# Performance work log

Measured on AMD Instinct MI355X. Metric: run time of the kernel, lower is better.

Reference implementation:

```python
import jax, jax.numpy as jnp
import numpy as np
import math

BS, LQ, LKV = 4, 2048, 2048
D_LATENT, D_MODEL, HEADS = 512, 512, 8
D_K = D_MODEL // HEADS


def setup_inputs() -> dict:
    key = jax.random.key(0)
    ks = jax.random.split(key, 12)
    s = 0.02
    return {
        "q": jax.random.normal(ks[0], (BS, LQ, D_LATENT), jnp.float32),
        "k": jax.random.normal(ks[1], (BS, LKV, D_MODEL), jnp.float32),
        "v": jax.random.normal(ks[2], (BS, LKV, D_MODEL), jnp.float32),
        "weights": jax.random.uniform(ks[3], (BS, LKV), jnp.float32) + 1e-3,
        "Wq": jax.random.normal(ks[4], (D_LATENT, D_MODEL), jnp.float32) * s,
        "bq": jnp.zeros((D_MODEL,), jnp.float32),
        "Wk": jax.random.normal(ks[5], (D_MODEL, D_MODEL), jnp.float32) * s,
        "bk": jnp.zeros((D_MODEL,), jnp.float32),
        "Wv": jax.random.normal(ks[6], (D_MODEL, D_MODEL), jnp.float32) * s,
        "bv": jnp.zeros((D_MODEL,), jnp.float32),
        "Wo": jax.random.normal(ks[7], (D_MODEL, D_MODEL), jnp.float32) * s,
        "bo": jnp.zeros((D_MODEL,), jnp.float32),
    }


def reference(q, k, v, weights, Wq, bq, Wk, bk, Wv, bv, Wo, bo):
    bs = q.shape[0]
    # QKV projections, split into heads: [bs, h, L, d_k]
    qh = (q @ Wq + bq).reshape(bs, -1, HEADS, D_K).transpose(0, 2, 1, 3)
    kh = (k @ Wk + bk).reshape(bs, -1, HEADS, D_K).transpose(0, 2, 1, 3)
    vh = (v @ Wv + bv).reshape(bs, -1, HEADS, D_K).transpose(0, 2, 1, 3)
    # scaled dot-product scores [bs, h, Lq, Lkv]
    scores = jnp.einsum("bhqd,bhkd->bhqk", qh, kh) / math.sqrt(D_K)
    p = jax.nn.softmax(scores, axis=-1)
    # post-softmax external weight renormalization
    wp = p * weights[:, None, None, :]
    wp = wp / wp.sum(-1, keepdims=True)
    out = jnp.einsum("bhqk,bhkd->bhqd", wp, vh)
    concat = out.transpose(0, 2, 1, 3).reshape(bs, -1, D_MODEL)
    return concat @ Wo + bo
```

## Files before the change

### kernel.cpp

```cpp
#include <hip/hip_runtime.h>
#include <hip/hip_bf16.h>

#define LQ 2048
#define LKV 2048
#define DM 512
#define NH 8
#define DK 64

typedef __attribute__((ext_vector_type(8))) __bf16 bf16x8;
typedef __attribute__((ext_vector_type(4))) float f32x4;
typedef __attribute__((ext_vector_type(16))) float f32x16;

#define AS1 __attribute__((address_space(1)))
#define AS3 __attribute__((address_space(3)))

static __device__ __forceinline__ unsigned short f2bf(float x) {
  unsigned u = __float_as_uint(x);
  return (unsigned short)((u + 0x7fffu + ((u >> 16) & 1u)) >> 16);
}
static __device__ __forceinline__ float bf2f(unsigned short u) {
  return __uint_as_float(((unsigned)u) << 16);
}
static __device__ __forceinline__ bf16x8 cvt8(f32x4 a, f32x4 b) {
  bf16x8 r;
  r[0] = (__bf16)a[0]; r[1] = (__bf16)a[1]; r[2] = (__bf16)a[2]; r[3] = (__bf16)a[3];
  r[4] = (__bf16)b[0]; r[5] = (__bf16)b[1]; r[6] = (__bf16)b[2]; r[7] = (__bf16)b[3];
  return r;
}

__global__ __launch_bounds__(256) void transpose_w(
    const float* __restrict__ Wq, const float* __restrict__ Wk,
    const float* __restrict__ Wv, const float* __restrict__ Wo,
    unsigned short* __restrict__ WtAll)
{
  const float* W = blockIdx.z == 0 ? Wq : blockIdx.z == 1 ? Wk : blockIdx.z == 2 ? Wv : Wo;
  unsigned short* Wt = WtAll + (size_t)blockIdx.z * DM * DM;
  __shared__ float tile[32][33];
  const int t = threadIdx.x;
  const int tr = t >> 3;
  const int tc4 = (t & 7) * 4;
  const int k0 = blockIdx.x * 32, n0 = blockIdx.y * 32;
  float4 v = *(const float4*)(W + (size_t)(k0 + tr) * DM + n0 + tc4);
  tile[tr][tc4 + 0] = v.x; tile[tr][tc4 + 1] = v.y;
  tile[tr][tc4 + 2] = v.z; tile[tr][tc4 + 3] = v.w;
  __syncthreads();
  ushort4 o;
  o.x = f2bf(tile[tc4 + 0][tr]);
  o.y = f2bf(tile[tc4 + 1][tr]);
  o.z = f2bf(tile[tc4 + 2][tr]);
  o.w = f2bf(tile[tc4 + 3][tr]);
  *(ushort4*)(Wt + (size_t)(n0 + tr) * DM + k0 + tc4) = o;
}

__global__ __launch_bounds__(256) void gemm_qkv(
    const float* __restrict__ qin, const float* __restrict__ kin, const float* __restrict__ vin,
    const unsigned short* __restrict__ WtAll,
    const float* __restrict__ bq, const float* __restrict__ bk, const float* __restrict__ bv,
    unsigned short* __restrict__ qh, unsigned short* __restrict__ kh, unsigned short* __restrict__ vh)
{
  const int bid = blockIdx.x;
  const int x = bid & 7, j = bid >> 3;
  const int p = x + 8 * (j >> 2);
  const int nt = j & 3;
  const int mode = p >> 6, mtile = p & 63;

  const float* A = mode == 0 ? qin : (mode == 1 ? kin : vin);
  const unsigned short* Bt = WtAll + (size_t)mode * DM * DM;
  const float* bias = mode == 0 ? bq : (mode == 1 ? bk : bv);
  unsigned short* out = mode == 0 ? qh : (mode == 1 ? kh : vh);
  const float scale = (mode == 0) ? 0.18033688011112042f : 1.0f;

  __shared__ __align__(16) float As[128 * 32];
  __shared__ __align__(16) unsigned short Bs[128 * 32];

  const int tid = threadIdx.x;
  const int lane = tid & 63;
  const int w = tid >> 6;
  const int wr = w >> 1, wc = w & 1;
  const int l15 = lane & 15, g = lane >> 4;
  const int m0 = mtile * 128, n0 = nt * 128;

  f32x4 acc[4][4] = {};

  for (int k0 = 0; k0 < DM; k0 += 32) {
#pragma unroll
    for (int i = 0; i < 4; ++i) {
      int c = tid + i * 256;
      int row = c >> 3, slot = c & 7;
      const float* src = A + (size_t)(m0 + row) * DM + k0 + ((slot ^ (row & 7)) << 2);
      __builtin_amdgcn_global_load_lds((const AS1 unsigned*)src,
                                       (AS3 unsigned*)((char*)As + c * 16), 16, 0, 0);
    }
#pragma unroll
    for (int i = 0; i < 2; ++i) {
      int c = tid + i * 256;
      int row = c >> 2, slot = c & 3;
      const unsigned short* src = Bt + (size_t)(n0 + row) * DM + k0 + ((slot ^ ((row >> 1) & 3)) * 8);
      __builtin_amdgcn_global_load_lds((const AS1 unsigned*)src,
                                       (AS3 unsigned*)((char*)Bs + c * 16), 16, 0, 0);
    }
    __syncthreads();

    bf16x8 af[4], bfr[4];
#pragma unroll
    for (int mi = 0; mi < 4; ++mi) {
      int row = wr * 64 + mi * 16 + l15;
      f32x4 a0 = *(const f32x4*)((const char*)As + row * 128 + (((2 * g) ^ (row & 7)) << 4));
      f32x4 a1 = *(const f32x4*)((const char*)As + row * 128 + (((2 * g + 1) ^ (row & 7)) << 4));
      af[mi] = cvt8(a0, a1);
    }
#pragma unroll
    for (int ni = 0; ni < 4; ++ni) {
      int row = wc * 64 + ni * 16 + l15;
      bfr[ni] = *(const bf16x8*)((const char*)Bs + row * 64 + ((g ^ ((row >> 1) & 3)) * 16));
    }
#pragma unroll
    for (int mi = 0; mi < 4; ++mi)
#pragma unroll
      for (int ni = 0; ni < 4; ++ni)
        acc[mi][ni] = __builtin_amdgcn_mfma_f32_16x16x32_bf16(af[mi], bfr[ni], acc[mi][ni], 0, 0, 0);
    __syncthreads();
  }

#pragma unroll
  for (int mi = 0; mi < 4; ++mi) {
#pragma unroll
    for (int ni = 0; ni < 4; ++ni) {
      int n = n0 + wc * 64 + ni * 16 + l15;
      float bs = bias[n];
      int h = n >> 6, d = n & 63;
#pragma unroll
      for (int r = 0; r < 4; ++r) {
        int m = m0 + wr * 64 + mi * 16 + g * 4 + r;
        int b = m >> 11, li = m & 2047;
        float val = (acc[mi][ni][r] + bs) * scale;
        out[(((size_t)(b * NH + h)) * LQ + li) * DK + d] = f2bf(val);
      }
    }
  }
}

__global__ __launch_bounds__(256) void gemm_out(
    const unsigned short* __restrict__ A, const unsigned short* __restrict__ Bt,
    const float* __restrict__ bias, float* __restrict__ out)
{
  __shared__ __align__(16) unsigned short Al[128 * 32];
  __shared__ __align__(16) unsigned short Bl[128 * 32];
  const int tid = threadIdx.x;
  const int lane = tid & 63;
  const int w = tid >> 6;
  const int wr = w >> 1, wc = w & 1;
  const int l15 = lane & 15, g = lane >> 4;
  const int m0 = blockIdx.x * 128, n0 = blockIdx.y * 128;
  f32x4 acc[4][4] = {};

  for (int k0 = 0; k0 < DM; k0 += 32) {
#pragma unroll
    for (int i = 0; i < 2; ++i) {
      int c = tid + i * 256;
      int row = c >> 2, slot = c & 3;
      int so = (slot ^ ((row >> 1) & 3)) * 8;
      __builtin_amdgcn_global_load_lds(
          (const AS1 unsigned*)(A + (size_t)(m0 + row) * DM + k0 + so),
          (AS3 unsigned*)((char*)Al + c * 16), 16, 0, 0);
      __builtin_amdgcn_global_load_lds(
          (const AS1 unsigned*)(Bt + (size_t)(n0 + row) * DM + k0 + so),
          (AS3 unsigned*)((char*)Bl + c * 16), 16, 0, 0);
    }
    __syncthreads();
    bf16x8 af[4], bfr[4];
#pragma unroll
    for (int mi = 0; mi < 4; ++mi) {
      int row = wr * 64 + mi * 16 + l15;
      af[mi] = *(const bf16x8*)((const char*)Al + row * 64 + ((g ^ ((row >> 1) & 3)) * 16));
    }
#pragma unroll
    for (int ni = 0; ni < 4; ++ni) {
      int row = wc * 64 + ni * 16 + l15;
      bfr[ni] = *(const bf16x8*)((const char*)Bl + row * 64 + ((g ^ ((row >> 1) & 3)) * 16));
    }
#pragma unroll
    for (int mi = 0; mi < 4; ++mi)
#pragma unroll
      for (int ni = 0; ni < 4; ++ni)
        acc[mi][ni] = __builtin_amdgcn_mfma_f32_16x16x32_bf16(af[mi], bfr[ni], acc[mi][ni], 0, 0, 0);
    __syncthreads();
  }

#pragma unroll
  for (int mi = 0; mi < 4; ++mi) {
#pragma unroll
    for (int ni = 0; ni < 4; ++ni) {
      int n = n0 + wc * 64 + ni * 16 + l15;
      float bs = bias[n];
#pragma unroll
      for (int r = 0; r < 4; ++r) {
        int m = m0 + wr * 64 + mi * 16 + g * 4 + r;
        out[(size_t)m * DM + n] = acc[mi][ni][r] + bs;
      }
    }
  }
}

__global__ __launch_bounds__(256) void prep_kv(
    const unsigned short* __restrict__ kh, const unsigned short* __restrict__ vh,
    const float* __restrict__ wts,
    unsigned short* __restrict__ kf, unsigned short* __restrict__ vf,
    unsigned short* __restrict__ wbf)
{
  __shared__ __align__(16) unsigned short t[64 * 72];
  const int bh = blockIdx.y, l0 = blockIdx.x * 64;
  const int b = bh >> 3;
  const size_t base = (size_t)bh * LKV * DK;
  const int tid = threadIdx.x;

  if ((bh & 7) == 0 && tid < 64) {
    int kv = l0 + tid;
    int r = kv & 15;
    int p = (r & 3) | ((r & 4) << 1) | ((r & 8) >> 1);
    wbf[b * LKV + (kv & ~15) + p] = f2bf(wts[b * LKV + kv]);
  }

#pragma unroll
  for (int i = 0; i < 2; ++i) {
    int c = tid + i * 256;
    int sl = c & 63, cq = (c >> 6) & 3, tl = c >> 8;
    int kv = tl * 32 + (sl & 31);
    int4 blk = *(const int4*)(kh + base + (size_t)(l0 + kv) * DK + cq * 16 + (sl >> 5) * 8);
    *(int4*)(kf + base + ((((size_t)(l0 >> 5) + tl) * 4 + cq) * 64 + sl) * 8) = blk;
  }

#pragma unroll
  for (int i = 0; i < 2; ++i) {
    int idx = tid + i * 256;
    int row = idx >> 3, seg = idx & 7;
    *(int4*)(&t[row * 72 + seg * 8]) =
        *(const int4*)(vh + base + (size_t)(l0 + row) * DK + seg * 8);
  }
  __syncthreads();
#pragma unroll
  for (int i = 0; i < 2; ++i) {
    int idx = tid + i * 256;
    int d = idx >> 3, seg = idx & 7;
    int kvg = l0 + seg * 8;
    float4 wa = *(const float4*)(wts + b * LKV + kvg);
    float4 wb4 = *(const float4*)(wts + b * LKV + kvg + 4);
    unsigned short r0 = f2bf(wa.x * bf2f(t[(seg * 8 + 0) * 72 + d]));
    unsigned short r1 = f2bf(wa.y * bf2f(t[(seg * 8 + 1) * 72 + d]));
    unsigned short r2 = f2bf(wa.z * bf2f(t[(seg * 8 + 2) * 72 + d]));
    unsigned short r3 = f2bf(wa.w * bf2f(t[(seg * 8 + 3) * 72 + d]));
    unsigned short r4 = f2bf(wb4.x * bf2f(t[(seg * 8 + 4) * 72 + d]));
    unsigned short r5 = f2bf(wb4.y * bf2f(t[(seg * 8 + 5) * 72 + d]));
    unsigned short r6 = f2bf(wb4.z * bf2f(t[(seg * 8 + 6) * 72 + d]));
    unsigned short r7 = f2bf(wb4.w * bf2f(t[(seg * 8 + 7) * 72 + d]));
    int T = kvg >> 4, s = (kvg >> 3) & 1, dh = d >> 5, dl = d & 31;
    size_t slot = (((size_t)bh * 128 + T) * 2 + dh) * 64;
    ushort4 lo4, hi4;
    lo4.x = r0; lo4.y = r1; lo4.z = r2; lo4.w = r3;
    hi4.x = r4; hi4.y = r5; hi4.z = r6; hi4.w = r7;
    *(ushort4*)(vf + (slot + dl) * 8 + 4 * s) = lo4;
    *(ushort4*)(vf + (slot + dl + 32) * 8 + 4 * s) = hi4;
  }
}

__global__ __launch_bounds__(512, 4) void attn_fwd(
    const unsigned short* __restrict__ qh, const unsigned short* __restrict__ kf,
    const unsigned short* __restrict__ vf, const unsigned short* __restrict__ wbf,
    unsigned short* __restrict__ ao)
{
  const int bid = blockIdx.x;
  const int xcd = bid & 7, wi = bid >> 3;
  const int bh = xcd * 4 + (wi >> 4);
  const int qb = wi & 15;
  const int b = bh >> 3, h = bh & 7;
  const int tid = threadIdx.x, lane = tid & 63, w = tid >> 6;
  const int wq = w & 3, half = w >> 2;
  const int l31 = lane & 31, hi = lane >> 5;

  __shared__ __align__(16) char smem[35328];

  const size_t kv_bh = (size_t)bh * (LKV * DK);
  const unsigned short* kfb = kf + kv_bh;
  const unsigned short* vfb = vf + kv_bh;

  const int q0 = qb * 128 + wq * 32;

#define STAGE(buf, t)                                                                     \
  do {                                                                                    \
    int tg_ = half * 32 + (t);                                                            \
    const unsigned short* ks_ = kfb + ((size_t)(tg_ * 4 + wq) * 64 + lane) * 8;           \
    char* kd_ = smem + (buf) * 8192 + half * 4096 + wq * 1024;                            \
    __builtin_amdgcn_global_load_lds((const AS1 unsigned*)ks_, (AS3 unsigned*)kd_, 16, 0, 0); \
  } while (0)

  if (tid < 256)
    __builtin_amdgcn_global_load_lds((const AS1 unsigned*)(wbf + b * LKV + tid * 8),
                                     (AS3 unsigned*)(smem + 16384 + tid * 16), 16, 0, 0);
  if (tid < 16) *(int*)(smem + 20480 + tid * 4) = 0;
  STAGE(0, 0);

  bf16x8 qf[4];
  {
    const unsigned short* qp = qh + kv_bh + (size_t)(q0 + l31) * DK + hi * 8;
#pragma unroll
    for (int cq = 0; cq < 4; ++cq) qf[cq] = *(const bf16x8*)(qp + cq * 16);
  }
  __syncthreads();

  const char* wl = smem + 16384 + half * 2048 + hi * 16;
  const char* zpad = smem + 20480;
  f32x16 accO0 = {}, accO1 = {}, accL = {};
  int cur = 0;

#pragma unroll 2
  for (int t = 0; t < 32; ++t) {
    const int tg = half * 32 + t;

    const unsigned short* vt_ = vfb + ((size_t)tg << 11) + lane * 8;
    bf16x8 vbr0 = *(const bf16x8*)(vt_);
    bf16x8 vbr1 = *(const bf16x8*)(vt_ + 512);
    bf16x8 vbr2 = *(const bf16x8*)(vt_ + 1024);
    bf16x8 vbr3 = *(const bf16x8*)(vt_ + 1536);

    if (t < 31) {
      STAGE(cur ^ 1, t + 1);
      asm volatile("s_waitcnt vmcnt(5)" ::: "memory");
    } else {
      asm volatile("s_waitcnt vmcnt(4)" ::: "memory");
    }
    __builtin_amdgcn_s_barrier();

    const char* Kb = smem + cur * 8192 + half * 4096;

    __builtin_amdgcn_s_setprio(1);
    f32x16 s = {};
#pragma unroll
    for (int cq = 0; cq < 4; ++cq) {
      bf16x8 kfr = *(const bf16x8*)(Kb + cq * 1024 + lane * 16);
      s = __builtin_amdgcn_mfma_f32_32x32x16_bf16(kfr, qf[cq], s, 0, 0, 0);
    }

    union { unsigned u[8]; bf16x8 v[2]; } P;
#pragma unroll
    for (int r2 = 0; r2 < 8; ++r2) {
      float lo = __builtin_amdgcn_exp2f(s[2 * r2]);
      float hv = __builtin_amdgcn_exp2f(s[2 * r2 + 1]);
      __bf16 bl = (__bf16)lo, bh2 = (__bf16)hv;
      unsigned short ul = __builtin_bit_cast(unsigned short, bl);
      unsigned short uh = __builtin_bit_cast(unsigned short, bh2);
      P.u[r2] = (unsigned)ul | ((unsigned)uh << 16);
    }

    const char* wsel = (l31 == 0) ? (wl + t * 64) : zpad;

    {
      bf16x8 wb0 = *(const bf16x8*)(wsel);
      bf16x8 wb1 = *(const bf16x8*)(wsel + 32);
      accO0 = __builtin_amdgcn_mfma_f32_32x32x16_bf16(P.v[0], vbr0, accO0, 0, 0, 0);
      accO1 = __builtin_amdgcn_mfma_f32_32x32x16_bf16(P.v[0], vbr1, accO1, 0, 0, 0);
      accL  = __builtin_amdgcn_mfma_f32_32x32x16_bf16(P.v[0], wb0,  accL,  0, 0, 0);
      accO0 = __builtin_amdgcn_mfma_f32_32x32x16_bf16(P.v[1], vbr2, accO0, 0, 0, 0);
      accO1 = __builtin_amdgcn_mfma_f32_32x32x16_bf16(P.v[1], vbr3, accO1, 0, 0, 0);
      accL  = __builtin_amdgcn_mfma_f32_32x32x16_bf16(P.v[1], wb1,  accL,  0, 0, 0);
    }
    __builtin_amdgcn_s_setprio(0);

    asm volatile("s_waitcnt lgkmcnt(0)" ::: "memory");
    __builtin_amdgcn_s_barrier();
    cur ^= 1;
  }
#undef STAGE

  float* Ob = (float*)smem;
  float* Lb = (float*)(smem + 34816);
  if (half == 1) {
#pragma unroll
    for (int r = 0; r < 16; ++r) {
      int qp_ = (r & 3) + 8 * (r >> 2) + 4 * hi;
      Ob[(wq * 32 + qp_) * 68 + l31] = accO0[r];
      Ob[(wq * 32 + qp_) * 68 + 32 + l31] = accO1[r];
    }
    if (l31 == 0) {
#pragma unroll
      for (int r = 0; r < 16; ++r) {
        int qp_ = (r & 3) + 8 * (r >> 2) + 4 * hi;
        Lb[wq * 32 + qp_] = accL[r];
      }
    }
  }
  __syncthreads();
  if (half == 0) {
#pragma unroll
    for (int r = 0; r < 16; ++r) {
      int qp_ = (r & 3) + 8 * (r >> 2) + 4 * hi;
      float L = __shfl(accL[r], lane & 32) + Lb[wq * 32 + qp_];
      float inv = 1.0f / L;
      float o0 = accO0[r] + Ob[(wq * 32 + qp_) * 68 + l31];
      float o1 = accO1[r] + Ob[(wq * 32 + qp_) * 68 + 32 + l31];
      size_t off = ((size_t)(b * LQ + q0 + qp_)) * DM + h * DK;
      ao[off + l31] = f2bf(o0 * inv);
      ao[off + 32 + l31] = f2bf(o1 * inv);
    }
  }
}

extern "C" void kernel_launch(void* const* d_in, const int* in_sizes, int n_in,
                              void* d_out, int out_size, void* d_ws, size_t ws_size,
                              hipStream_t stream)
{
  const float* q  = (const float*)d_in[0];
  const float* k  = (const float*)d_in[1];
  const float* v  = (const float*)d_in[2];
  const float* wt = (const float*)d_in[3];
  const float* Wq = (const float*)d_in[4];
  const float* bq = (const float*)d_in[5];
  const float* Wk = (const float*)d_in[6];
  const float* bk = (const float*)d_in[7];
  const float* Wv = (const float*)d_in[8];
  const float* bv = (const float*)d_in[9];
  const float* Wo = (const float*)d_in[10];
  const float* bo = (const float*)d_in[11];

  char* ws = (char*)d_ws;
  unsigned short* qh = (unsigned short*)(ws + 0);
  unsigned short* kfr= (unsigned short*)(ws + 8388608);
  unsigned short* vfr= (unsigned short*)(ws + 16777216);
  unsigned short* ao = (unsigned short*)(ws + 25165824);
  unsigned short* Wt = (unsigned short*)(ws + 33554432);
  unsigned short* vh = (unsigned short*)(ws + 35651584);
  unsigned short* wbf= (unsigned short*)(ws + 44040192);
  unsigned short* kh = ao;

  transpose_w<<<dim3(16, 16, 4), 256, 0, stream>>>(Wq, Wk, Wv, Wo, Wt);
  gemm_qkv<<<768, 256, 0, stream>>>(q, k, v, Wt, bq, bk, bv, qh, kh, vh);
  prep_kv<<<dim3(32, 32), 256, 0, stream>>>(kh, vh, wt, kfr, vfr, wbf);
  attn_fwd<<<512, 512, 0, stream>>>(qh, kfr, vfr, wbf, ao);
  gemm_out<<<dim3(64, 4), 256, 0, stream>>>(ao, Wt + 3 * (size_t)DM * DM, bo, (float*)d_out);
}
```

Before: 96.21 us.

## Process two query tiles per wave and stage V through LDS

Each attention block now uses 4 waves of 256 threads instead of 8, and each wave handles 64 query rows as two 32-row groups that share the K and V fragments read from LDS. V tiles are now loaded asynchronously into double-buffered shared memory alongside K, replacing the per-wave direct global register loads. This cuts redundant K/V traffic per query and overlaps V loads with compute. The cost is double the accumulator registers per wave, fewer waves to hide latency, and a larger shared-memory footprint.

```diff
diff --git a/kernel.cpp b/kernel.cpp
--- a/kernel.cpp
+++ b/kernel.cpp
@@ -263,7 +263,7 @@
   }
 }
 
-__global__ __launch_bounds__(512, 4) void attn_fwd(
+__global__ __launch_bounds__(256, 2) void attn_fwd(
     const unsigned short* __restrict__ qh, const unsigned short* __restrict__ kf,
     const unsigned short* __restrict__ vf, const unsigned short* __restrict__ wbf,
     unsigned short* __restrict__ ao)
@@ -274,94 +274,101 @@
   const int qb = wi & 15;
   const int b = bh >> 3, h = bh & 7;
   const int tid = threadIdx.x, lane = tid & 63, w = tid >> 6;
-  const int wq = w & 3, half = w >> 2;
+  const int wq = w & 1, half = w >> 1;
   const int l31 = lane & 31, hi = lane >> 5;
 
-  __shared__ __align__(16) char smem[35328];
+  __shared__ __align__(16) char smem[36928];
 
   const size_t kv_bh = (size_t)bh * (LKV * DK);
   const unsigned short* kfb = kf + kv_bh;
   const unsigned short* vfb = vf + kv_bh;
 
-  const int q0 = qb * 128 + wq * 32;
+  const int q0 = qb * 128 + wq * 64;
 
 #define STAGE(buf, t)                                                                     \
   do {                                                                                    \
     int tg_ = half * 32 + (t);                                                            \
-    const unsigned short* ks_ = kfb + ((size_t)(tg_ * 4 + wq) * 64 + lane) * 8;           \
-    char* kd_ = smem + (buf) * 8192 + half * 4096 + wq * 1024;                            \
-    __builtin_amdgcn_global_load_lds((const AS1 unsigned*)ks_, (AS3 unsigned*)kd_, 16, 0, 0); \
+    _Pragma("unroll")                                                                     \
+    for (int j_ = 0; j_ < 2; ++j_) {                                                      \
+      int ch_ = wq * 2 + j_;                                                              \
+      const unsigned short* ks_ = kfb + ((size_t)(tg_ * 4 + ch_) * 64 + lane) * 8;        \
+      const unsigned short* vs_ = vfb + ((size_t)(tg_ * 4 + ch_) * 64 + lane) * 8;        \
+      char* kd_ = smem + (buf) * 8192 + half * 4096 + ch_ * 1024;                         \
+      char* vd_ = smem + 16384 + (buf) * 8192 + half * 4096 + ch_ * 1024;                 \
+      __builtin_amdgcn_global_load_lds((const AS1 unsigned*)ks_, (AS3 unsigned*)kd_, 16, 0, 0); \
+      __builtin_amdgcn_global_load_lds((const AS1 unsigned*)vs_, (AS3 unsigned*)vd_, 16, 0, 0); \
+    }                                                                                     \
   } while (0)
 
-  if (tid < 256)
-    __builtin_amdgcn_global_load_lds((const AS1 unsigned*)(wbf + b * LKV + tid * 8),
-                                     (AS3 unsigned*)(smem + 16384 + tid * 16), 16, 0, 0);
-  if (tid < 16) *(int*)(smem + 20480 + tid * 4) = 0;
+  __builtin_amdgcn_global_load_lds((const AS1 unsigned*)(wbf + b * LKV + tid * 8),
+                                   (AS3 unsigned*)(smem + 32768 + tid * 16), 16, 0, 0);
+  if (tid < 16) *(int*)(smem + 36864 + tid * 4) = 0;
   STAGE(0, 0);
 
-  bf16x8 qf[4];
+  bf16x8 qf0[4], qf1[4];
   {
     const unsigned short* qp = qh + kv_bh + (size_t)(q0 + l31) * DK + hi * 8;
 #pragma unroll
-    for (int cq = 0; cq < 4; ++cq) qf[cq] = *(const bf16x8*)(qp + cq * 16);
-  }
-  __syncthreads();
-
-  const char* wl = smem + 16384 + half * 2048 + hi * 16;
-  const char* zpad = smem + 20480;
-  f32x16 accO0 = {}, accO1 = {}, accL = {};
+    for (int cq = 0; cq < 4; ++cq) {
+      qf0[cq] = *(const bf16x8*)(qp + cq * 16);
+      qf1[cq] = *(const bf16x8*)(qp + 32 * DK + cq * 16);
+    }
+  }
+  asm volatile("s_waitcnt vmcnt(0) lgkmcnt(0)" ::: "memory");
+  __builtin_amdgcn_s_barrier();
+
+  const char* wl = smem + 32768 + half * 2048 + hi * 16;
+  const char* zpad = smem + 36864;
+  f32x16 aO0g0 = {}, aO1g0 = {}, aLg0 = {};
+  f32x16 aO0g1 = {}, aO1g1 = {}, aLg1 = {};
   int cur = 0;
 
-#pragma unroll 2
   for (int t = 0; t < 32; ++t) {
-    const int tg = half * 32 + t;
-
-    const unsigned short* vt_ = vfb + ((size_t)tg << 11) + lane * 8;
-    bf16x8 vbr0 = *(const bf16x8*)(vt_);
-    bf16x8 vbr1 = *(const bf16x8*)(vt_ + 512);
-    bf16x8 vbr2 = *(const bf16x8*)(vt_ + 1024);
-    bf16x8 vbr3 = *(const bf16x8*)(vt_ + 1536);
-
     if (t < 31) {
       STAGE(cur ^ 1, t + 1);
-      asm volatile("s_waitcnt vmcnt(5)" ::: "memory");
+      asm volatile("s_waitcnt vmcnt(4)" ::: "memory");
     } else {
-      asm volatile("s_waitcnt vmcnt(4)" ::: "memory");
+      asm volatile("s_waitcnt vmcnt(0)" ::: "memory");
     }
     __builtin_amdgcn_s_barrier();
 
     const char* Kb = smem + cur * 8192 + half * 4096;
+    const char* Vb = smem + 16384 + cur * 8192 + half * 4096;
 
     __builtin_amdgcn_s_setprio(1);
-    f32x16 s = {};
+    f32x16 s0 = {}, s1 = {};
 #pragma unroll
     for (int cq = 0; cq < 4; ++cq) {
       bf16x8 kfr = *(const bf16x8*)(Kb + cq * 1024 + lane * 16);
-      s = __builtin_amdgcn_mfma_f32_32x32x16_bf16(kfr, qf[cq], s, 0, 0, 0);
-    }
-
-    union { unsigned u[8]; bf16x8 v[2]; } P;
+      s0 = __builtin_amdgcn_mfma_f32_32x32x16_bf16(kfr, qf0[cq], s0, 0, 0, 0);
+      s1 = __builtin_amdgcn_mfma_f32_32x32x16_bf16(kfr, qf1[cq], s1, 0, 0, 0);
+    }
+
+    union { unsigned u[8]; bf16x8 v[2]; } P0, P1;
 #pragma unroll
     for (int r2 = 0; r2 < 8; ++r2) {
-      float lo = __builtin_amdgcn_exp2f(s[2 * r2]);
-      float hv = __builtin_amdgcn_exp2f(s[2 * r2 + 1]);
-      __bf16 bl = (__bf16)lo, bh2 = (__bf16)hv;
-      unsigned short ul = __builtin_bit_cast(unsigned short, bl);
-      unsigned short uh = __builtin_bit_cast(unsigned short, bh2);
-      P.u[r2] = (unsigned)ul | ((unsigned)uh << 16);
+      float a0 = __builtin_amdgcn_exp2f(s0[2 * r2]);
+      float a1 = __builtin_amdgcn_exp2f(s0[2 * r2 + 1]);
+      float b0 = __builtin_amdgcn_exp2f(s1[2 * r2]);
+      float b1 = __builtin_amdgcn_exp2f(s1[2 * r2 + 1]);
+      unsigned short ua0 = f2bf(a0), ua1 = f2bf(a1), ub0 = f2bf(b0), ub1 = f2bf(b1);
+      P0.u[r2] = (unsigned)ua0 | ((unsigned)ua1 << 16);
+      P1.u[r2] = (unsigned)ub0 | ((unsigned)ub1 << 16);
     }
 
     const char* wsel = (l31 == 0) ? (wl + t * 64) : zpad;
 
-    {
-      bf16x8 wb0 = *(const bf16x8*)(wsel);
-      bf16x8 wb1 = *(const bf16x8*)(wsel + 32);
-      accO0 = __builtin_amdgcn_mfma_f32_32x32x16_bf16(P.v[0], vbr0, accO0, 0, 0, 0);
-      accO1 = __builtin_amdgcn_mfma_f32_32x32x16_bf16(P.v[0], vbr1, accO1, 0, 0, 0);
-      accL  = __builtin_amdgcn_mfma_f32_32x32x16_bf16(P.v[0], wb0,  accL,  0, 0, 0);
-      accO0 = __builtin_amdgcn_mfma_f32_32x32x16_bf16(P.v[1], vbr2, accO0, 0, 0, 0);
-      accO1 = __builtin_amdgcn_mfma_f32_32x32x16_bf16(P.v[1], vbr3, accO1, 0, 0, 0);
-      accL  = __builtin_amdgcn_mfma_f32_32x32x16_bf16(P.v[1], wb1,  accL,  0, 0, 0);
+#pragma unroll
+    for (int c = 0; c < 2; ++c) {
+      bf16x8 vb0 = *(const bf16x8*)(Vb + (c * 2 + 0) * 1024 + lane * 16);
+      bf16x8 vb1 = *(const bf16x8*)(Vb + (c * 2 + 1) * 1024 + lane * 16);
+      bf16x8 wb = *(const bf16x8*)(wsel + c * 32);
+      aO0g0 = __builtin_amdgcn_mfma_f32_32x32x16_bf16(P0.v[c], vb0, aO0g0, 0, 0, 0);
+      aO1g0 = __builtin_amdgcn_mfma_f32_32x32x16_bf16(P0.v[c], vb1, aO1g0, 0, 0, 0);
+      aLg0  = __builtin_amdgcn_mfma_f32_32x32x16_bf16(P0.v[c], wb,  aLg0,  0, 0, 0);
+      aO0g1 = __builtin_amdgcn_mfma_f32_32x32x16_bf16(P1.v[c], vb0, aO0g1, 0, 0, 0);
+      aO1g1 = __builtin_amdgcn_mfma_f32_32x32x16_bf16(P1.v[c], vb1, aO1g1, 0, 0, 0);
+      aLg1  = __builtin_amdgcn_mfma_f32_32x32x16_bf16(P1.v[c], wb,  aLg1,  0, 0, 0);
     }
     __builtin_amdgcn_s_setprio(0);
 
@@ -377,14 +384,18 @@
 #pragma unroll
     for (int r = 0; r < 16; ++r) {
       int qp_ = (r & 3) + 8 * (r >> 2) + 4 * hi;
-      Ob[(wq * 32 + qp_) * 68 + l31] = accO0[r];
-      Ob[(wq * 32 + qp_) * 68 + 32 + l31] = accO1[r];
+      int row0 = wq * 64 + qp_, row1 = wq * 64 + 32 + qp_;
+      Ob[row0 * 68 + l31] = aO0g0[r];
+      Ob[row0 * 68 + 32 + l31] = aO1g0[r];
+      Ob[row1 * 68 + l31] = aO0g1[r];
+      Ob[row1 * 68 + 32 + l31] = aO1g1[r];
     }
     if (l31 == 0) {
 #pragma unroll
       for (int r = 0; r < 16; ++r) {
         int qp_ = (r & 3) + 8 * (r >> 2) + 4 * hi;
-        Lb[wq * 32 + qp_] = accL[r];
+        Lb[wq * 64 + qp_] = aLg0[r];
+        Lb[wq * 64 + 32 + qp_] = aLg1[r];
       }
     }
   }
@@ -393,13 +404,26 @@
 #pragma unroll
     for (int r = 0; r < 16; ++r) {
       int qp_ = (r & 3) + 8 * (r >> 2) + 4 * hi;
-      float L = __shfl(accL[r], lane & 32) + Lb[wq * 32 + qp_];
-      float inv = 1.0f / L;
-      float o0 = accO0[r] + Ob[(wq * 32 + qp_) * 68 + l31];
-      float o1 = accO1[r] + Ob[(wq * 32 + qp_) * 68 + 32 + l31];
-      size_t off = ((size_t)(b * LQ + q0 + qp_)) * DM + h * DK;
-      ao[off + l31] = f2bf(o0 * inv);
-      ao[off + 32 + l31] = f2bf(o1 * inv);
+      {
+        int row = wq * 64 + qp_;
+        float L = __shfl(aLg0[r], lane & 32) + Lb[row];
+        float inv = 1.0f / L;
+        float o0 = aO0g0[r] + Ob[row * 68 + l31];
+        float o1 = aO1g0[r] + Ob[row * 68 + 32 + l31];
+        size_t off = ((size_t)(b * LQ + q0 + qp_)) * DM + h * DK;
+        ao[off + l31] = f2bf(o0 * inv);
+        ao[off + 32 + l31] = f2bf(o1 * inv);
+      }
+      {
+        int row = wq * 64 + 32 + qp_;
+        float L = __shfl(aLg1[r], lane & 32) + Lb[row];
+        float inv = 1.0f / L;
+        float o0 = aO0g1[r] + Ob[row * 68 + l31];
+        float o1 = aO1g1[r] + Ob[row * 68 + 32 + l31];
+        size_t off = ((size_t)(b * LQ + q0 + 32 + qp_)) * DM + h * DK;
+        ao[off + l31] = f2bf(o0 * inv);
+        ao[off + 32 + l31] = f2bf(o1 * inv);
+      }
     }
   }
 }
@@ -434,6 +458,6 @@
   transpose_w<<<dim3(16, 16, 4), 256, 0, stream>>>(Wq, Wk, Wv, Wo, Wt);
   gemm_qkv<<<768, 256, 0, stream>>>(q, k, v, Wt, bq, bk, bv, qh, kh, vh);
   prep_kv<<<dim3(32, 32), 256, 0, stream>>>(kh, vh, wt, kfr, vfr, wbf);
-  attn_fwd<<<512, 512, 0, stream>>>(qh, kfr, vfr, wbf, ao);
+  attn_fwd<<<512, 256, 0, stream>>>(qh, kfr, vfr, wbf, ao);
   gemm_out<<<dim3(64, 4), 256, 0, stream>>>(ao, Wt + 3 * (size_t)DM * DM, bo, (float*)d_out);
 }
```

After: 98.12 us. About the same (+2.0%).
